# Optimization experiments

Measured on AMD Instinct MI355X. Metric: run time of the kernel, lower is better.

The kernel has to match this reference:

```python
import jax, jax.numpy as jnp
import numpy as np
from functools import partial

HIDDEN = 96
D_STATE = 16
D_CONV = 3
EXPAND = 2
D_INNER = EXPAND * HIDDEN            # 192
DT_RANK = -(-D_INNER // 16)          # ceil(192/16) = 12
B_SZ, H_SP, W_SP = 16, 64, 64


def setup_inputs() -> dict:
    key = jax.random.key(0)
    ks = jax.random.split(key, 12)
    def w(k, shape, fan_in):
        return jax.random.normal(k, shape, dtype=jnp.float32) * (fan_in ** -0.5)
    di = D_INNER
    inp = {
        "x": jax.random.normal(ks[0], (B_SZ, HIDDEN, H_SP, W_SP), dtype=jnp.float32),
        "in_proj_w": w(ks[1], (2 * di, HIDDEN), HIDDEN),
        "conv2d_w": w(ks[2], (di, 1, D_CONV, D_CONV), D_CONV * D_CONV),
        "m_in_proj_w": w(ks[3], (2 * di, di), di),
        "m_conv1d_w": w(ks[4], (di, 1, D_CONV), D_CONV),
        "m_conv1d_b": jnp.zeros((di,), dtype=jnp.float32),
        "m_x_proj_w": w(ks[5], (DT_RANK + 2 * D_STATE, di), di),
        "m_dt_proj_w": w(ks[6], (di, DT_RANK), DT_RANK),
        "m_dt_proj_b": jax.random.uniform(ks[7], (di,), dtype=jnp.float32, minval=-4.0, maxval=-2.0),
        "m_A_log": jnp.log(jnp.tile(jnp.arange(1, D_STATE + 1, dtype=jnp.float32)[None, :], (di, 1))),
        "m_D": jnp.ones((di,), dtype=jnp.float32),
        "m_out_proj_w": w(ks[8], (di, di), di),
        "out_proj_w": w(ks[9], (HIDDEN, di), di),
    }
    return inp


def _mamba(u, in_w, c1_w, c1_b, xp_w, dt_w, dt_b, A_log, Dp, out_w):
    # u: [B, L, di] -> [B, L, di]
    Bn, L, di = u.shape
    xz = jnp.einsum("bld,ed->ble", u, in_w)          # [B,L,2di]
    xm, z = jnp.split(xz, 2, axis=-1)
    # causal depthwise conv1d (torch pads k-1 then truncates to L)
    xc = jax.lax.conv_general_dilated(
        xm.transpose(0, 2, 1), c1_w, window_strides=(1,),
        padding=[(D_CONV - 1, 0)], feature_group_count=di,
        dimension_numbers=("NCH", "OIH", "NCH"))
    xm = jax.nn.silu(xc + c1_b[None, :, None]).transpose(0, 2, 1)  # [B,L,di]
    dbl = jnp.einsum("bld,ed->ble", xm, xp_w)         # [B,L,dt_rank+2N]
    dt_r = dbl[..., :DT_RANK]
    Bm = dbl[..., DT_RANK:DT_RANK + D_STATE]
    Cm = dbl[..., DT_RANK + D_STATE:]
    dt = jax.nn.softplus(jnp.einsum("blr,dr->bld", dt_r, dt_w) + dt_b)  # [B,L,di]
    A = -jnp.exp(A_log)                               # [di, N]

    def step(h, inp):
        dt_t, x_t, B_t, C_t = inp                     # [B,di],[B,di],[B,N],[B,N]
        da = jnp.exp(dt_t[..., None] * A)             # [B,di,N]
        h = da * h + (dt_t * x_t)[..., None] * B_t[:, None, :]
        y = jnp.einsum("bdn,bn->bd", h, C_t)
        return h, y

    xs = (dt.transpose(1, 0, 2), xm.transpose(1, 0, 2),
          Bm.transpose(1, 0, 2), Cm.transpose(1, 0, 2))
    h0 = jnp.zeros((Bn, di, D_STATE), dtype=u.dtype)
    _, ys = jax.lax.scan(step, h0, xs)                # ys: [L,B,di]
    y = ys.transpose(1, 0, 2) + xm * Dp
    y = y * jax.nn.silu(z)
    return jnp.einsum("bld,ed->ble", y, out_w)


def reference(x, in_proj_w, conv2d_w, m_in_proj_w, m_conv1d_w, m_conv1d_b,
              m_x_proj_w, m_dt_proj_w, m_dt_proj_b, m_A_log, m_D,
              m_out_proj_w, out_proj_w):
    B, C, H, W = x.shape
    di = D_INNER
    xp = x.transpose(0, 2, 3, 1)                      # [B,H,W,C]
    xz = jnp.einsum("bhwc,ec->bhwe", xp, in_proj_w)   # [B,H,W,2di]
    x_in, x_gate = jnp.split(xz, 2, axis=-1)
    xc = jax.lax.conv_general_dilated(
        x_in.transpose(0, 3, 1, 2), conv2d_w, window_strides=(1, 1),
        padding="SAME", feature_group_count=di,
        dimension_numbers=("NCHW", "OIHW", "NCHW"))
    x_act = jax.nn.silu(xc).transpose(0, 2, 3, 1).reshape(B, H * W, di)
    ym = _mamba(x_act, m_in_proj_w, m_conv1d_w, m_conv1d_b, m_x_proj_w,
                m_dt_proj_w, m_dt_proj_b, m_A_log, m_D, m_out_proj_w)
    ym = ym.reshape(B, H, W, di) * jax.nn.silu(x_gate)
    out = jnp.einsum("bhwd,cd->bhwc", ym, out_proj_w)
    return out.transpose(0, 3, 1, 2)                  # [B,C,H,W]
```

## Files before the change

kernel.cpp:

```cpp
#include <hip/hip_runtime.h>
#include <hip/hip_bf16.h>

#define DI   192
#define DS   16
#define LSEQ 4096
#define NB   16
#define NCH  128
#define CHL  32

typedef unsigned short u16;
typedef __bf16 bfrag   __attribute__((ext_vector_type(8)));
typedef unsigned short u16x8 __attribute__((ext_vector_type(8)));
typedef float f32x4    __attribute__((ext_vector_type(4)));
typedef float f32x2    __attribute__((ext_vector_type(2)));

__device__ __forceinline__ float silu_f(float x) {
    return x * __builtin_amdgcn_rcpf(1.f + __expf(-x));
}
__device__ __forceinline__ float bf2f(u16 u) {
    return __uint_as_float(((unsigned)u) << 16);
}
__device__ __forceinline__ u16 f2bf(float f) {
    unsigned u = __float_as_uint(f);
    return (u16)((u + 0x7FFFu + ((u >> 16) & 1u)) >> 16);
}
__device__ __forceinline__ u16 f2h(float f) {
    return __builtin_bit_cast(u16, (_Float16)f);
}
__device__ __forceinline__ float h2f(u16 u) {
    return (float)__builtin_bit_cast(_Float16, u);
}

template<int E>
__device__ __forceinline__ long pkidx(long bt, int e) {
    return (((bt >> 4) * (E / 32) + (e >> 5)) * 64
            + ((int)bt & 15) + (((e >> 3) & 3) << 4)) * 8 + (e & 7);
}

__device__ __forceinline__ void fma8(float (&acc)[8], const float4& wa,
                                     const float4& wb, const u16x8& v) {
    acc[0] = fmaf(wa.x, bf2f(v[0]), acc[0]);
    acc[1] = fmaf(wa.y, bf2f(v[1]), acc[1]);
    acc[2] = fmaf(wa.z, bf2f(v[2]), acc[2]);
    acc[3] = fmaf(wa.w, bf2f(v[3]), acc[3]);
    acc[4] = fmaf(wb.x, bf2f(v[4]), acc[4]);
    acc[5] = fmaf(wb.y, bf2f(v[5]), acc[5]);
    acc[6] = fmaf(wb.z, bf2f(v[6]), acc[6]);
    acc[7] = fmaf(wb.w, bf2f(v[7]), acc[7]);
}

template<int K, bool GATED, int OUTMODE>
__global__ __launch_bounds__(256) void gemm_pk(
    const u16* __restrict__ A, const u16* __restrict__ G,
    const u16* __restrict__ Wp,
    u16* __restrict__ ob0, u16* __restrict__ ob1,
    float* __restrict__ of, int E)
{
    __shared__ u16 Cs[64][72];
    const int tid  = threadIdx.x;
    const int lane = tid & 63, wv = tid >> 6;
    const int b  = blockIdx.z;
    const int tB = blockIdx.x * 64;
    const int e0 = blockIdx.y * 64;
    const int r16 = lane & 15, kg = lane >> 4;
    const int mo = (wv >> 1) * 32, no = (wv & 1) * 32;
    constexpr int KB = K / 32;

    f32x4 acc00 = {0.f, 0.f, 0.f, 0.f};
    f32x4 acc01 = acc00, acc10 = acc00, acc11 = acc00;

    const long Tg = ((long)b * LSEQ + tB + mo) >> 4;
    const u16* ap0 = A + Tg * (KB * 512) + lane * 8;
    const u16* ap1 = ap0 + KB * 512;
    const u16* wp0 = Wp + (long)((e0 + no) >> 4) * (KB * 512) + lane * 8;
    const u16* wp1 = wp0 + KB * 512;
    const u16* gp0 = nullptr; const u16* gp1 = nullptr;
    if constexpr (GATED) {
        gp0 = G + Tg * (KB * 512) + lane * 8;
        gp1 = gp0 + KB * 512;
    }

    #pragma unroll
    for (int ks = 0; ks < KB; ++ks) {
        bfrag a0, a1, b0, b1;
        if constexpr (GATED) {
            u16x8 y0 = *(const u16x8*)(ap0 + ks * 512);
            u16x8 y1 = *(const u16x8*)(ap1 + ks * 512);
            u16x8 g0 = *(const u16x8*)(gp0 + ks * 512);
            u16x8 g1 = *(const u16x8*)(gp1 + ks * 512);
            u16x8 p0, p1;
            #pragma unroll
            for (int j = 0; j < 8; ++j) {
                p0[j] = f2bf(bf2f(y0[j]) * silu_f(bf2f(g0[j])));
                p1[j] = f2bf(bf2f(y1[j]) * silu_f(bf2f(g1[j])));
            }
            a0 = __builtin_bit_cast(bfrag, p0);
            a1 = __builtin_bit_cast(bfrag, p1);
        } else {
            a0 = *(const bfrag*)(ap0 + ks * 512);
            a1 = *(const bfrag*)(ap1 + ks * 512);
        }
        b0 = *(const bfrag*)(wp0 + ks * 512);
        b1 = *(const bfrag*)(wp1 + ks * 512);
        acc00 = __builtin_amdgcn_mfma_f32_16x16x32_bf16(a0, b0, acc00, 0, 0, 0);
        acc01 = __builtin_amdgcn_mfma_f32_16x16x32_bf16(a0, b1, acc01, 0, 0, 0);
        acc10 = __builtin_amdgcn_mfma_f32_16x16x32_bf16(a1, b0, acc10, 0, 0, 0);
        acc11 = __builtin_amdgcn_mfma_f32_16x16x32_bf16(a1, b1, acc11, 0, 0, 0);
    }

    if constexpr (OUTMODE == 0) {
        #pragma unroll
        for (int m = 0; m < 2; ++m) {
            const f32x4 am0 = m ? acc10 : acc00;
            const f32x4 am1 = m ? acc11 : acc01;
            long t0 = (long)b * LSEQ + tB + mo + m * 16 + kg * 4;
            int c0 = e0 + no + r16, c1 = e0 + no + 16 + r16;
            #pragma unroll
            for (int i = 0; i < 4; ++i) {
                if (c0 < E) of[(t0 + i) * E + c0] = am0[i];
                if (c1 < E) of[(t0 + i) * E + c1] = am1[i];
            }
        }
    } else if constexpr (OUTMODE == 1) {
        #pragma unroll
        for (int m = 0; m < 2; ++m) {
            const f32x4 am0 = m ? acc10 : acc00;
            const f32x4 am1 = m ? acc11 : acc01;
            int rr = mo + m * 16 + kg * 4;
            #pragma unroll
            for (int i = 0; i < 4; ++i) {
                Cs[rr + i][no + r16]      = f2bf(am0[i]);
                Cs[rr + i][no + 16 + r16] = f2bf(am1[i]);
            }
        }
        __syncthreads();
        int row = tid >> 2, q = tid & 3;
        long bt = (long)b * LSEQ + tB + row;
        u16x8 v0 = *(const u16x8*)&Cs[row][q * 16];
        u16x8 v1 = *(const u16x8*)&Cs[row][q * 16 + 8];
        int eg = e0 + q * 16;
        if (eg < 192) {
            *(u16x8*)&ob0[pkidx<192>(bt, eg)]     = v0;
            *(u16x8*)&ob0[pkidx<192>(bt, eg + 8)] = v1;
        } else {
            *(u16x8*)&ob1[pkidx<192>(bt, eg - 192)]     = v0;
            *(u16x8*)&ob1[pkidx<192>(bt, eg - 184)]     = v1;
        }
    } else {
        #pragma unroll
        for (int m = 0; m < 2; ++m) {
            const f32x4 am0 = m ? acc10 : acc00;
            const f32x4 am1 = m ? acc11 : acc01;
            long tt = tB + mo + m * 16 + kg * 4;
            int c0 = e0 + no + r16, c1 = e0 + no + 16 + r16;
            if (c0 < E) {
                float4 v = make_float4(am0[0], am0[1], am0[2], am0[3]);
                *(float4*)&of[((long)b * E + c0) * LSEQ + tt] = v;
            }
            if (c1 < E) {
                float4 v = make_float4(am1[0], am1[1], am1[2], am1[3]);
                *(float4*)&of[((long)b * E + c1) * LSEQ + tt] = v;
            }
        }
    }
}

#define DECAY_PAIRS(rr)                                                    \
    float rr2s = (rr) * (rr);                                              \
    float rr4 = rr2s * rr2s;                                               \
    float rr8 = rr4 * rr4;                                                 \
    f32x2 r2v = {rr2s, rr2s}, r4v = {rr4, rr4}, r8v = {rr8, rr8};          \
    f32x2 p0 = {(rr), rr2s};                                               \
    f32x2 p1 = p0 * r2v;                                                   \
    f32x2 p2 = p0 * r4v;                                                   \
    f32x2 p3 = p1 * r4v;                                                   \
    f32x2 p4 = p0 * r8v;                                                   \
    f32x2 p5 = p1 * r8v;                                                   \
    f32x2 p6 = p2 * r8v;                                                   \
    f32x2 p7 = p3 * r8v;

__global__ __launch_bounds__(384) void xproj_dt_scanA(
    const u16* __restrict__ XC, const u16* __restrict__ Wp,
    const float* __restrict__ WTdt, const float* __restrict__ Bdt,
    float* __restrict__ DBLo, u16* __restrict__ DT,
    float* __restrict__ Sdt, float* __restrict__ CH)
{
    __shared__ float Ds[64][46];
    __shared__ u16 dtS[64][192];
    const int tid  = threadIdx.x;
    const int lane = tid & 63, wv = tid >> 6;
    const int b  = blockIdx.z;
    const int tB = blockIdx.x * 64;
    const long bt0 = (long)b * LSEQ + tB;
    constexpr int KB = 6;

    if (wv < 4) {
        const int r16 = lane & 15, kg = lane >> 4;
        const int mo = (wv >> 1) * 32, no = (wv & 1) * 32;
        f32x4 acc00 = {0.f, 0.f, 0.f, 0.f};
        f32x4 acc01 = acc00, acc10 = acc00, acc11 = acc00;
        const long Tg = (bt0 + mo) >> 4;
        const u16* ap0 = XC + Tg * (KB * 512) + lane * 8;
        const u16* ap1 = ap0 + KB * 512;
        const u16* wp0 = Wp + (long)(no >> 4) * (KB * 512) + lane * 8;
        const u16* wp1 = wp0 + KB * 512;
        #pragma unroll
        for (int ks = 0; ks < KB; ++ks) {
            bfrag a0 = *(const bfrag*)(ap0 + ks * 512);
            bfrag a1 = *(const bfrag*)(ap1 + ks * 512);
            bfrag b0 = *(const bfrag*)(wp0 + ks * 512);
            bfrag b1 = *(const bfrag*)(wp1 + ks * 512);
            acc00 = __builtin_amdgcn_mfma_f32_16x16x32_bf16(a0, b0, acc00, 0, 0, 0);
            acc01 = __builtin_amdgcn_mfma_f32_16x16x32_bf16(a0, b1, acc01, 0, 0, 0);
            acc10 = __builtin_amdgcn_mfma_f32_16x16x32_bf16(a1, b0, acc10, 0, 0, 0);
            acc11 = __builtin_amdgcn_mfma_f32_16x16x32_bf16(a1, b1, acc11, 0, 0, 0);
        }
        #pragma unroll
        for (int m = 0; m < 2; ++m) {
            const f32x4 am0 = m ? acc10 : acc00;
            const f32x4 am1 = m ? acc11 : acc01;
            int row0 = mo + m * 16 + kg * 4;
            int c0 = no + r16, c1 = no + 16 + r16;
            #pragma unroll
            for (int i = 0; i < 4; ++i) {
                if (c0 < 44) {
                    Ds[row0 + i][c0] = am0[i];
                    if (c0 >= 12) DBLo[(bt0 + row0 + i) * 44 + c0] = am0[i];
                }
                if (c1 < 44) {
                    Ds[row0 + i][c1] = am1[i];
                    if (c1 >= 12) DBLo[(bt0 + row0 + i) * 44 + c1] = am1[i];
                }
            }
        }
    }
    __syncthreads();

    #pragma unroll
    for (int u = 0; u < 4; ++u) {
        int i = tid + u * 384;
        int t = i / 24, dblk = i % 24;
        int d0 = dblk * 8;
        const float4 b0 = *(const float4*)&Bdt[d0];
        const float4 b1 = *(const float4*)&Bdt[d0 + 4];
        float s[8] = {b0.x, b0.y, b0.z, b0.w, b1.x, b1.y, b1.z, b1.w};
        #pragma unroll
        for (int k = 0; k < 12; ++k) {
            float rv = Ds[t][k];
            const float4 wa = *(const float4*)&WTdt[k * DI + d0];
            const float4 wb = *(const float4*)&WTdt[k * DI + d0 + 4];
            s[0] = fmaf(wa.x, rv, s[0]);
            s[1] = fmaf(wa.y, rv, s[1]);
            s[2] = fmaf(wa.z, rv, s[2]);
            s[3] = fmaf(wa.w, rv, s[3]);
            s[4] = fmaf(wb.x, rv, s[4]);
            s[5] = fmaf(wb.y, rv, s[5]);
            s[6] = fmaf(wb.z, rv, s[6]);
            s[7] = fmaf(wb.w, rv, s[7]);
        }
        u16x8 o;
        #pragma unroll
        for (int j = 0; j < 8; ++j) {
            float e = __expf(s[j]);
            float dtv = (s[j] > 20.f) ? s[j] : __logf(1.f + e);
            o[j] = f2h(dtv);
        }
        *(u16x8*)&dtS[t][d0] = o;
        *(u16x8*)&DT[pkidx<192>(bt0 + t, d0)] = o;
    }
    __syncthreads();

    const int chunk = tid / 192;
    const int d = tid - chunk * 192;
    const int c = blockIdx.x * 2 + chunk;
    const long btc = bt0 + chunk * CHL;
    const long baseT = (btc >> 4) * 3072;
    const int doff = (d >> 5) * 512 + ((d >> 3) & 3) * 128 + (d & 7);
    f32x2 h2[8];
    #pragma unroll
    for (int n = 0; n < 8; ++n) h2[n] = (f32x2){0.f, 0.f};
    float sumdt = 0.f;
    for (int l = 0; l < CHL; ++l) {
        int tok = chunk * CHL + l;
        float dtv = h2f(dtS[tok][d]);
        float xv  = bf2f(XC[baseT + ((l >> 4) * 3072) + ((l & 15) << 3) + doff]);
        float rr = __expf(-dtv);
        sumdt += dtv;
        float dx = dtv * xv;
        DECAY_PAIRS(rr)
        const f32x2* brow = (const f32x2*)(&Ds[tok][12]);
        f32x2 dx2 = {dx, dx};
        h2[0] = p0 * h2[0] + dx2 * brow[0];
        h2[1] = p1 * h2[1] + dx2 * brow[1];
        h2[2] = p2 * h2[2] + dx2 * brow[2];
        h2[3] = p3 * h2[3] + dx2 * brow[3];
        h2[4] = p4 * h2[4] + dx2 * brow[4];
        h2[5] = p5 * h2[5] + dx2 * brow[5];
        h2[6] = p6 * h2[6] + dx2 * brow[6];
        h2[7] = p7 * h2[7] + dx2 * brow[7];
    }
    Sdt[((long)b * NCH + c) * DI + d] = sumdt;
    long co = (long)(b * NCH + c) * DS * DI + d;
    #pragma unroll
    for (int n = 0; n < 8; ++n) {
        CH[co + (long)(2 * n) * DI]     = h2[n].x;
        CH[co + (long)(2 * n + 1) * DI] = h2[n].y;
    }
}

__device__ __forceinline__ void pack_one(
    u16* __restrict__ dst, const float* __restrict__ src,
    int srcE, int K, int i)
{
    int j = i & 7, lane = (i >> 3) & 63, blk = i >> 9;
    int kb = blk % (K / 32), T = blk / (K / 32);
    int e = T * 16 + (lane & 15);
    int k = kb * 32 + (lane >> 4) * 8 + j;
    dst[i] = (e < srcE) ? f2bf(src[e * K + k]) : (u16)0;
}

__global__ __launch_bounds__(256) void cvt_w(
    const float* __restrict__ s_in, const float* __restrict__ s_min,
    const float* __restrict__ s_xp, const float* __restrict__ s_om,
    const float* __restrict__ s_out, const float* __restrict__ s_c2,
    const float* __restrict__ s_c1, const float* __restrict__ s_dt,
    u16* __restrict__ d_in_, u16* __restrict__ d_min_, u16* __restrict__ d_xp_,
    u16* __restrict__ d_om_, u16* __restrict__ d_out_,
    float* __restrict__ d_c2t, float* __restrict__ d_c1t,
    float* __restrict__ d_dtt)
{
    int i = blockIdx.x * 256 + threadIdx.x;
    if      (i < 36864)  pack_one(d_in_,  s_in,  384, 96,  i);
    else if (i < 110592) pack_one(d_min_, s_min, 384, 192, i - 36864);
    else if (i < 122880) pack_one(d_xp_,  s_xp,  44,  192, i - 110592);
    else if (i < 159744) pack_one(d_om_,  s_om,  192, 192, i - 122880);
    else if (i < 184320) pack_one(d_out_, s_out, 96,  192, i - 159744);
    else if (i < 186048) {
        int j = i - 184320; int d = j / 9, k = j % 9;
        d_c2t[k * DI + d] = s_c2[j];
    } else if (i < 186624) {
        int j = i - 186048; int d = j / 3, k = j % 3;
        d_c1t[k * DI + d] = s_c1[j];
    } else if (i < 188928) {
        int j = i - 186624; int d = j / 12, k = j % 12;
        d_dtt[k * DI + d] = s_dt[j];
    }
}

__global__ __launch_bounds__(256) void xpose_x(
    const float* __restrict__ X, u16* __restrict__ XT)
{
    __shared__ u16 T[128][96];
    const int tid = threadIdx.x;
    const int t0 = blockIdx.x * 128, b = blockIdx.y;
    for (int lin = tid; lin < 128 * 96; lin += 256) {
        int k = lin / 128, t = lin % 128;
        T[t][k] = f2bf(X[((long)b * 96 + k) * LSEQ + t0 + t]);
    }
    __syncthreads();
    for (int lin = tid; lin < 128 * 12; lin += 256) {
        int t = lin / 12, seg = lin % 12;
        *(u16x8*)&XT[pkidx<96>((long)b * LSEQ + t0 + t, seg * 8)] =
            *(const u16x8*)&T[t][seg * 8];
    }
}

__global__ __launch_bounds__(256) void conv2d_silu(
    const u16* __restrict__ X, const float* __restrict__ WT, u16* __restrict__ O)
{
    int q8 = (int)(gridDim.x >> 3);
    int sbid = ((int)blockIdx.x & 7) * q8 + ((int)blockIdx.x >> 3);
    long idx = (long)sbid * 256 + threadIdx.x;
    int dblk = (int)(idx % 24);  long r = idx / 24;
    int w4 = (int)(r & 15); r >>= 4;
    int h  = (int)(r & 63); r >>= 6;
    int b  = (int)r;
    int w0 = w4 * 4;
    int d0 = dblk * 8;
    long bbase = (long)b * LSEQ;
    float acc[4][8] = {{0.f}};
    const u16x8 zv = {0,0,0,0,0,0,0,0};
    #pragma unroll
    for (int kh = 0; kh < 3; ++kh) {
        int hh = h + kh - 1;
        if (hh < 0 || hh > 63) continue;
        long rowt = bbase + hh * 64;
        u16x8 v0 = (w0 >= 1)  ? *(const u16x8*)&X[pkidx<192>(rowt + w0 - 1, d0)] : zv;
        u16x8 v1 = *(const u16x8*)&X[pkidx<192>(rowt + w0,     d0)];
        u16x8 v2 = *(const u16x8*)&X[pkidx<192>(rowt + w0 + 1, d0)];
        u16x8 v3 = *(const u16x8*)&X[pkidx<192>(rowt + w0 + 2, d0)];
        u16x8 v4 = *(const u16x8*)&X[pkidx<192>(rowt + w0 + 3, d0)];
        u16x8 v5 = (w0 <= 59) ? *(const u16x8*)&X[pkidx<192>(rowt + w0 + 4, d0)] : zv;
        #pragma unroll
        for (int kw = 0; kw < 3; ++kw) {
            const float4 wa = *(const float4*)&WT[(kh * 3 + kw) * DI + d0];
            const float4 wb = *(const float4*)&WT[(kh * 3 + kw) * DI + d0 + 4];
            if (kw == 0) { fma8(acc[0], wa, wb, v0); fma8(acc[1], wa, wb, v1);
                           fma8(acc[2], wa, wb, v2); fma8(acc[3], wa, wb, v3); }
            if (kw == 1) { fma8(acc[0], wa, wb, v1); fma8(acc[1], wa, wb, v2);
                           fma8(acc[2], wa, wb, v3); fma8(acc[3], wa, wb, v4); }
            if (kw == 2) { fma8(acc[0], wa, wb, v2); fma8(acc[1], wa, wb, v3);
                           fma8(acc[2], wa, wb, v4); fma8(acc[3], wa, wb, v5); }
        }
    }
    #pragma unroll
    for (int o = 0; o < 4; ++o) {
        u16x8 ov;
        #pragma unroll
        for (int j = 0; j < 8; ++j) ov[j] = f2bf(silu_f(acc[o][j]));
        *(u16x8*)&O[pkidx<192>(bbase + h * 64 + w0 + o, d0)] = ov;
    }
}

__global__ __launch_bounds__(256) void conv1d_silu(
    const u16* __restrict__ XM, const float* __restrict__ WT,
    const float* __restrict__ Bc, u16* __restrict__ XC)
{
    long idx = (long)blockIdx.x * 256 + threadIdx.x;
    int dblk = (int)(idx % 24);  long r = idx / 24;
    int l4 = (int)(r & 1023); r >>= 10;
    int b  = (int)r;
    int l0 = l4 * 4;
    int d0 = dblk * 8;
    long bbase = (long)b * LSEQ;
    const float4 ba = *(const float4*)&Bc[d0];
    const float4 bb = *(const float4*)&Bc[d0 + 4];
    float acc[4][8];
    #pragma unroll
    for (int o = 0; o < 4; ++o) {
        acc[o][0]=ba.x; acc[o][1]=ba.y; acc[o][2]=ba.z; acc[o][3]=ba.w;
        acc[o][4]=bb.x; acc[o][5]=bb.y; acc[o][6]=bb.z; acc[o][7]=bb.w;
    }
    const u16x8 zv = {0,0,0,0,0,0,0,0};
    u16x8 v0 = (l0 >= 2) ? *(const u16x8*)&XM[pkidx<192>(bbase + l0 - 2, d0)] : zv;
    u16x8 v1 = (l0 >= 1) ? *(const u16x8*)&XM[pkidx<192>(bbase + l0 - 1, d0)] : zv;
    u16x8 v2 = *(const u16x8*)&XM[pkidx<192>(bbase + l0,     d0)];
    u16x8 v3 = *(const u16x8*)&XM[pkidx<192>(bbase + l0 + 1, d0)];
    u16x8 v4 = *(const u16x8*)&XM[pkidx<192>(bbase + l0 + 2, d0)];
    u16x8 v5 = *(const u16x8*)&XM[pkidx<192>(bbase + l0 + 3, d0)];
    #pragma unroll
    for (int k = 0; k < 3; ++k) {
        const float4 wa = *(const float4*)&WT[k * DI + d0];
        const float4 wb = *(const float4*)&WT[k * DI + d0 + 4];
        if (k == 0) { fma8(acc[0], wa, wb, v0); fma8(acc[1], wa, wb, v1);
                      fma8(acc[2], wa, wb, v2); fma8(acc[3], wa, wb, v3); }
        if (k == 1) { fma8(acc[0], wa, wb, v1); fma8(acc[1], wa, wb, v2);
                      fma8(acc[2], wa, wb, v3); fma8(acc[3], wa, wb, v4); }
        if (k == 2) { fma8(acc[0], wa, wb, v2); fma8(acc[1], wa, wb, v3);
                      fma8(acc[2], wa, wb, v4); fma8(acc[3], wa, wb, v5); }
    }
    #pragma unroll
    for (int o = 0; o < 4; ++o) {
        u16x8 ov;
        #pragma unroll
        for (int j = 0; j < 8; ++j) ov[j] = f2bf(silu_f(acc[o][j]));
        *(u16x8*)&XC[pkidx<192>(bbase + l0 + o, d0)] = ov;
    }
}

#define SC_ADDR(l) (baseT + ((l) >> 4) * 3072 + (((l) & 15) << 3) + doff)

__global__ __launch_bounds__(256) void scan_pass_b(
    const float* __restrict__ Sdt, const float* __restrict__ Alog, float* CH)
{
    int idx = blockIdx.x * 256 + threadIdx.x;
    int d = idx % DI;
    int n = (idx / DI) % DS;
    int b = idx / (DI * DS);
    float A = -__expf(Alog[d * DS + n]);
    float hs = 0.f;
    #pragma unroll 8
    for (int c = 0; c < NCH; ++c) {
        float P = __expf(A * Sdt[((long)b * NCH + c) * DI + d]);
        long off = ((long)(b * NCH + c) * DS + n) * DI + d;
        float hloc = CH[off];
        CH[off] = hs;
        hs = fmaf(P, hs, hloc);
    }
}

__global__ __launch_bounds__(192) void scan_pass_c(
    const u16* __restrict__ XC, const u16* __restrict__ DT,
    const float* __restrict__ DBLp, const float* __restrict__ Dpar,
    const float* __restrict__ HIN, u16* __restrict__ Y)
{
    const int c = blockIdx.x, b = blockIdx.y, d = threadIdx.x;
    __shared__ float BCs[CHL][32];
    long bt0 = (long)b * LSEQ + c * CHL;
    long baseT = (bt0 >> 4) * 3072;
    int doff = (d >> 5) * 512 + ((d >> 3) & 3) * 128 + (d & 7);
    for (int lin = d; lin < CHL * 32; lin += 192) {
        int l = lin >> 5, j = lin & 31;
        BCs[l][j] = DBLp[(bt0 + l) * 44 + 12 + j];
    }
    f32x2 h2[8];
    long co = (long)(b * NCH + c) * DS * DI + d;
    #pragma unroll
    for (int n = 0; n < 8; ++n) {
        h2[n].x = HIN[co + (long)(2 * n) * DI];
        h2[n].y = HIN[co + (long)(2 * n + 1) * DI];
    }
    float Dv = Dpar[d];
    __syncthreads();
    for (int l = 0; l < CHL; ++l) {
        float dtv = h2f(DT[SC_ADDR(l)]);
        float xv  = bf2f(XC[SC_ADDR(l)]);
        float rr = __expf(-dtv);
        float dx = dtv * xv;
        DECAY_PAIRS(rr)
        const f32x2* brow = (const f32x2*)(&BCs[l][0]);
        f32x2 dx2 = {dx, dx};
        f32x2 ya = {0.f, 0.f}, yb = {0.f, 0.f};
        h2[0] = p0 * h2[0] + dx2 * brow[0];
        h2[1] = p1 * h2[1] + dx2 * brow[1];
        ya = h2[0] * brow[8]  + ya;
        yb = h2[1] * brow[9]  + yb;
        h2[2] = p2 * h2[2] + dx2 * brow[2];
        h2[3] = p3 * h2[3] + dx2 * brow[3];
        ya = h2[2] * brow[10] + ya;
        yb = h2[3] * brow[11] + yb;
        h2[4] = p4 * h2[4] + dx2 * brow[4];
        h2[5] = p5 * h2[5] + dx2 * brow[5];
        ya = h2[4] * brow[12] + ya;
        yb = h2[5] * brow[13] + yb;
        h2[6] = p6 * h2[6] + dx2 * brow[6];
        h2[7] = p7 * h2[7] + dx2 * brow[7];
        ya = h2[6] * brow[14] + ya;
        yb = h2[7] * brow[15] + yb;
        f32x2 ys = ya + yb;
        float y = ys.x + ys.y;
        y = fmaf(xv, Dv, y);
        Y[SC_ADDR(l)] = f2bf(y);
    }
}

extern "C" void kernel_launch(void* const* d_in, const int* in_sizes, int n_in,
                              void* d_out, int out_size, void* d_ws, size_t ws_size,
                              hipStream_t stream)
{
    const float* x     = (const float*)d_in[0];
    const float* w_in  = (const float*)d_in[1];
    const float* w_c2  = (const float*)d_in[2];
    const float* w_min = (const float*)d_in[3];
    const float* w_c1  = (const float*)d_in[4];
    const float* b_c1  = (const float*)d_in[5];
    const float* w_xp  = (const float*)d_in[6];
    const float* w_dt  = (const float*)d_in[7];
    const float* b_dt  = (const float*)d_in[8];
    const float* alog  = (const float*)d_in[9];
    const float* Dpar  = (const float*)d_in[10];
    const float* w_om  = (const float*)d_in[11];
    const float* w_out = (const float*)d_in[12];
    float* out = (float*)d_out;

    const long NTD = (long)NB * LSEQ * DI;
    char* p = (char*)d_ws;
    u16* WP_in  = (u16*)p; p += 36864 * 2;
    u16* WP_min = (u16*)p; p += 73728 * 2;
    u16* WP_xp  = (u16*)p; p += 12288 * 2;
    u16* WP_om  = (u16*)p; p += 36864 * 2;
    u16* WP_out = (u16*)p; p += 24576 * 2;
    float* WT2  = (float*)p; p += 1728 * 4;
    float* WT1  = (float*)p; p += 576 * 4;
    float* WTdt = (float*)p; p += 2304 * 4;
    u16* XT = (u16*)p; p += (long)NB * LSEQ * 96 * 2;
    u16* B1 = (u16*)p; p += NTD * 2;
    u16* B2 = (u16*)p; p += NTD * 2;
    u16* B3 = (u16*)p; p += NTD * 2;
    u16* B4 = (u16*)p; p += NTD * 2;
    u16* B5 = (u16*)p; p += NTD * 2;
    float* DBL = (float*)p; p += (long)NB * LSEQ * 44 * 4;
    float* Sdt = (float*)p; p += (long)NB * NCH * DI * 4;
    float* CH  = (float*)p; p += (long)NB * NCH * DS * DI * 4;

    dim3 blk(256);
    int nblk4  = (int)((long)NB * LSEQ * 24 / 4 / 256);

    cvt_w<<<738, blk, 0, stream>>>(w_in, w_min, w_xp, w_om, w_out, w_c2, w_c1,
                                   w_dt, WP_in, WP_min, WP_xp, WP_om, WP_out,
                                   WT2, WT1, WTdt);
    xpose_x<<<dim3(32, NB), blk, 0, stream>>>(x, XT);
    gemm_pk<96, false, 1><<<dim3(64, 6, NB), blk, 0, stream>>>(
        XT, nullptr, WP_in, B1, B2, nullptr, 384);
    conv2d_silu<<<nblk4, blk, 0, stream>>>(B1, WT2, B3);
    gemm_pk<192, false, 1><<<dim3(64, 6, NB), blk, 0, stream>>>(
        B3, nullptr, WP_min, B5, B4, nullptr, 384);
    conv1d_silu<<<nblk4, blk, 0, stream>>>(B5, WT1, b_c1, B3);
    xproj_dt_scanA<<<dim3(64, 1, NB), dim3(384), 0, stream>>>(
        B3, WP_xp, WTdt, b_dt, DBL, B1, Sdt, CH);
    scan_pass_b<<<dim3(192), blk, 0, stream>>>(Sdt, alog, CH);
    scan_pass_c<<<dim3(NCH, NB), dim3(192), 0, stream>>>(B3, B1, DBL, Dpar, CH, B5);
    gemm_pk<192, true, 1><<<dim3(64, 3, NB), blk, 0, stream>>>(
        B5, B4, WP_om, B1, nullptr, nullptr, 192);
    gemm_pk<192, true, 2><<<dim3(64, 2, NB), blk, 0, stream>>>(
        B1, B2, WP_out, nullptr, nullptr, out, 96);
}
```

Measured before the change: 240.5 us.

## Fold local scan output into pass A and replace pass C with a decay correction

The first scan pass now also computes each chunk's local output y, including the C contraction and the D skip term. It writes that output along with a per-token cumulative dt in fp16, instead of writing dt itself. The final pass no longer reruns the state recurrence. It adds a correction term to y: the incoming chunk state, decayed by exp(-cumdt) raised to the per-state powers, dotted with C. This removes the recomputation and the x/dt reads in the last pass. In exchange, pass A does more arithmetic, y is read, modified and written back in bf16, and cumulative dt stored in fp16 can lose precision.

```diff
diff --git a/kernel.cpp b/kernel.cpp
--- a/kernel.cpp
+++ b/kernel.cpp
@@ -182,8 +182,9 @@
 __global__ __launch_bounds__(384) void xproj_dt_scanA(
     const u16* __restrict__ XC, const u16* __restrict__ Wp,
     const float* __restrict__ WTdt, const float* __restrict__ Bdt,
-    float* __restrict__ DBLo, u16* __restrict__ DT,
-    float* __restrict__ Sdt, float* __restrict__ CH)
+    const float* __restrict__ Dpar,
+    float* __restrict__ DBLo, u16* __restrict__ CD,
+    u16* __restrict__ Y, float* __restrict__ Sdt, float* __restrict__ CH)
 {
     __shared__ float Ds[64][46];
     __shared__ u16 dtS[64][192];
@@ -225,11 +226,11 @@
             for (int i = 0; i < 4; ++i) {
                 if (c0 < 44) {
                     Ds[row0 + i][c0] = am0[i];
-                    if (c0 >= 12) DBLo[(bt0 + row0 + i) * 44 + c0] = am0[i];
+                    if (c0 >= 28) DBLo[(bt0 + row0 + i) * 44 + c0] = am0[i];
                 }
                 if (c1 < 44) {
                     Ds[row0 + i][c1] = am1[i];
-                    if (c1 >= 12) DBLo[(bt0 + row0 + i) * 44 + c1] = am1[i];
+                    if (c1 >= 28) DBLo[(bt0 + row0 + i) * 44 + c1] = am1[i];
                 }
             }
         }
@@ -266,7 +267,6 @@
             o[j] = f2h(dtv);
         }
         *(u16x8*)&dtS[t][d0] = o;
-        *(u16x8*)&DT[pkidx<192>(bt0 + t, d0)] = o;
     }
     __syncthreads();
 
@@ -276,35 +276,94 @@
     const long btc = bt0 + chunk * CHL;
     const long baseT = (btc >> 4) * 3072;
     const int doff = (d >> 5) * 512 + ((d >> 3) & 3) * 128 + (d & 7);
+    const float Dv = Dpar[d];
     f32x2 h2[8];
     #pragma unroll
     for (int n = 0; n < 8; ++n) h2[n] = (f32x2){0.f, 0.f};
-    float sumdt = 0.f;
+    float cumdt = 0.f;
     for (int l = 0; l < CHL; ++l) {
         int tok = chunk * CHL + l;
+        long addr = baseT + ((l >> 4) * 3072) + ((l & 15) << 3) + doff;
         float dtv = h2f(dtS[tok][d]);
-        float xv  = bf2f(XC[baseT + ((l >> 4) * 3072) + ((l & 15) << 3) + doff]);
+        float xv  = bf2f(XC[addr]);
         float rr = __expf(-dtv);
-        sumdt += dtv;
+        cumdt += dtv;
         float dx = dtv * xv;
         DECAY_PAIRS(rr)
         const f32x2* brow = (const f32x2*)(&Ds[tok][12]);
+        const f32x2* crow = (const f32x2*)(&Ds[tok][28]);
         f32x2 dx2 = {dx, dx};
+        f32x2 ya = {0.f, 0.f}, yb = {0.f, 0.f};
         h2[0] = p0 * h2[0] + dx2 * brow[0];
         h2[1] = p1 * h2[1] + dx2 * brow[1];
+        ya = h2[0] * crow[0] + ya;
+        yb = h2[1] * crow[1] + yb;
         h2[2] = p2 * h2[2] + dx2 * brow[2];
         h2[3] = p3 * h2[3] + dx2 * brow[3];
+        ya = h2[2] * crow[2] + ya;
+        yb = h2[3] * crow[3] + yb;
         h2[4] = p4 * h2[4] + dx2 * brow[4];
         h2[5] = p5 * h2[5] + dx2 * brow[5];
+        ya = h2[4] * crow[4] + ya;
+        yb = h2[5] * crow[5] + yb;
         h2[6] = p6 * h2[6] + dx2 * brow[6];
         h2[7] = p7 * h2[7] + dx2 * brow[7];
-    }
-    Sdt[((long)b * NCH + c) * DI + d] = sumdt;
+        ya = h2[6] * crow[6] + ya;
+        yb = h2[7] * crow[7] + yb;
+        f32x2 ys = ya + yb;
+        float y = ys.x + ys.y;
+        y = fmaf(xv, Dv, y);
+        Y[addr]  = f2bf(y);
+        CD[addr] = f2h(cumdt);
+    }
+    Sdt[((long)b * NCH + c) * DI + d] = cumdt;
     long co = (long)(b * NCH + c) * DS * DI + d;
     #pragma unroll
     for (int n = 0; n < 8; ++n) {
         CH[co + (long)(2 * n) * DI]     = h2[n].x;
         CH[co + (long)(2 * n + 1) * DI] = h2[n].y;
+    }
+}
+
+__global__ __launch_bounds__(192) void corr_pass(
+    const u16* __restrict__ CD, const float* __restrict__ DBLp,
+    const float* __restrict__ HIN, u16* Y)
+{
+    const int c = blockIdx.x, b = blockIdx.y, d = threadIdx.x;
+    __shared__ float Ccs[CHL][16];
+    long bt0 = (long)b * LSEQ + c * CHL;
+    long baseT = (bt0 >> 4) * 3072;
+    int doff = (d >> 5) * 512 + ((d >> 3) & 3) * 128 + (d & 7);
+    for (int lin = d; lin < CHL * 16; lin += 192) {
+        int l = lin >> 4, j = lin & 15;
+        Ccs[l][j] = DBLp[(bt0 + l) * 44 + 28 + j];
+    }
+    f32x2 h2[8];
+    long co = (long)(b * NCH + c) * DS * DI + d;
+    #pragma unroll
+    for (int n = 0; n < 8; ++n) {
+        h2[n].x = HIN[co + (long)(2 * n) * DI];
+        h2[n].y = HIN[co + (long)(2 * n + 1) * DI];
+    }
+    __syncthreads();
+    for (int l = 0; l < CHL; ++l) {
+        long addr = baseT + ((l >> 4) * 3072) + ((l & 15) << 3) + doff;
+        float cum = h2f(CD[addr]);
+        float rr = __expf(-cum);
+        DECAY_PAIRS(rr)
+        const f32x2* crow = (const f32x2*)(&Ccs[l][0]);
+        f32x2 ya, yb;
+        ya = (p0 * h2[0]) * crow[0];
+        yb = (p1 * h2[1]) * crow[1];
+        ya = (p2 * h2[2]) * crow[2] + ya;
+        yb = (p3 * h2[3]) * crow[3] + yb;
+        ya = (p4 * h2[4]) * crow[4] + ya;
+        yb = (p5 * h2[5]) * crow[5] + yb;
+        ya = (p6 * h2[6]) * crow[6] + ya;
+        yb = (p7 * h2[7]) * crow[7] + yb;
+        f32x2 ys = ya + yb;
+        float corr = ys.x + ys.y;
+        Y[addr] = f2bf(bf2f(Y[addr]) + corr);
     }
 }
 
@@ -458,8 +517,6 @@
     }
 }
 
-#define SC_ADDR(l) (baseT + ((l) >> 4) * 3072 + (((l) & 15) << 3) + doff)
-
 __global__ __launch_bounds__(256) void scan_pass_b(
     const float* __restrict__ Sdt, const float* __restrict__ Alog, float* CH)
 {
@@ -476,61 +533,6 @@
         float hloc = CH[off];
         CH[off] = hs;
         hs = fmaf(P, hs, hloc);
-    }
-}
-
-__global__ __launch_bounds__(192) void scan_pass_c(
-    const u16* __restrict__ XC, const u16* __restrict__ DT,
-    const float* __restrict__ DBLp, const float* __restrict__ Dpar,
-    const float* __restrict__ HIN, u16* __restrict__ Y)
-{
-    const int c = blockIdx.x, b = blockIdx.y, d = threadIdx.x;
-    __shared__ float BCs[CHL][32];
-    long bt0 = (long)b * LSEQ + c * CHL;
-    long baseT = (bt0 >> 4) * 3072;
-    int doff = (d >> 5) * 512 + ((d >> 3) & 3) * 128 + (d & 7);
-    for (int lin = d; lin < CHL * 32; lin += 192) {
-        int l = lin >> 5, j = lin & 31;
-        BCs[l][j] = DBLp[(bt0 + l) * 44 + 12 + j];
-    }
-    f32x2 h2[8];
-    long co = (long)(b * NCH + c) * DS * DI + d;
-    #pragma unroll
-    for (int n = 0; n < 8; ++n) {
-        h2[n].x = HIN[co + (long)(2 * n) * DI];
-        h2[n].y = HIN[co + (long)(2 * n + 1) * DI];
-    }
-    float Dv = Dpar[d];
-    __syncthreads();
-    for (int l = 0; l < CHL; ++l) {
-        float dtv = h2f(DT[SC_ADDR(l)]);
-        float xv  = bf2f(XC[SC_ADDR(l)]);
-        float rr = __expf(-dtv);
-        float dx = dtv * xv;
-        DECAY_PAIRS(rr)
-        const f32x2* brow = (const f32x2*)(&BCs[l][0]);
-        f32x2 dx2 = {dx, dx};
-        f32x2 ya = {0.f, 0.f}, yb = {0.f, 0.f};
-        h2[0] = p0 * h2[0] + dx2 * brow[0];
-        h2[1] = p1 * h2[1] + dx2 * brow[1];
-        ya = h2[0] * brow[8]  + ya;
-        yb = h2[1] * brow[9]  + yb;
-        h2[2] = p2 * h2[2] + dx2 * brow[2];
-        h2[3] = p3 * h2[3] + dx2 * brow[3];
-        ya = h2[2] * brow[10] + ya;
-        yb = h2[3] * brow[11] + yb;
-        h2[4] = p4 * h2[4] + dx2 * brow[4];
-        h2[5] = p5 * h2[5] + dx2 * brow[5];
-        ya = h2[4] * brow[12] + ya;
-        yb = h2[5] * brow[13] + yb;
-        h2[6] = p6 * h2[6] + dx2 * brow[6];
-        h2[7] = p7 * h2[7] + dx2 * brow[7];
-        ya = h2[6] * brow[14] + ya;
-        yb = h2[7] * brow[15] + yb;
-        f32x2 ys = ya + yb;
-        float y = ys.x + ys.y;
-        y = fmaf(xv, Dv, y);
-        Y[SC_ADDR(l)] = f2bf(y);
     }
 }
 
@@ -587,9 +589,9 @@
         B3, nullptr, WP_min, B5, B4, nullptr, 384);
     conv1d_silu<<<nblk4, blk, 0, stream>>>(B5, WT1, b_c1, B3);
     xproj_dt_scanA<<<dim3(64, 1, NB), dim3(384), 0, stream>>>(
-        B3, WP_xp, WTdt, b_dt, DBL, B1, Sdt, CH);
+        B3, WP_xp, WTdt, b_dt, Dpar, DBL, B1, B5, Sdt, CH);
     scan_pass_b<<<dim3(192), blk, 0, stream>>>(Sdt, alog, CH);
-    scan_pass_c<<<dim3(NCH, NB), dim3(192), 0, stream>>>(B3, B1, DBL, Dpar, CH, B5);
+    corr_pass<<<dim3(NCH, NB), dim3(192), 0, stream>>>(B1, DBL, CH, B5);
     gemm_pk<192, true, 1><<<dim3(64, 3, NB), blk, 0, stream>>>(
         B5, B4, WP_om, B1, nullptr, nullptr, 192);
     gemm_pk<192, true, 2><<<dim3(64, 2, NB), blk, 0, stream>>>(
```

After: 246.6 us. 1.03x slower.
